# Optimization experiments

Measured on AMD Instinct MI355X. Metric: run time of the kernel, lower is better.

Reference implementation:

```python
import jax, jax.numpy as jnp
import numpy as np

N_NODES = 30000
N_EDGES = 480000
NODE_DIM = 16
NUM_RADIAL = 8
NUM_ELEMENTS = 120
R_MAX = 5.0
NUM_BLOCKS = 2
N_PATHS = 5  # h0*sh0->0e, h0*sh1->1o, h0*sh2->2e, h1.sh1->0e, h2.sh2->0e


def _sh_basis(u):
    # real spherical harmonics up to l=2, component normalization, on unit vectors u [E,3]
    x, y, z = u[:, 0], u[:, 1], u[:, 2]
    s15 = jnp.sqrt(jnp.asarray(15.0, u.dtype))
    s5 = jnp.sqrt(jnp.asarray(5.0, u.dtype))
    sh1 = jnp.sqrt(jnp.asarray(3.0, u.dtype)) * u                      # [E,3]
    sh2 = jnp.stack([s15 * x * y, s15 * y * z,
                     0.5 * s5 * (3.0 * z * z - 1.0),
                     s15 * x * z, 0.5 * s15 * (x * x - y * y)], -1)    # [E,5]
    return sh1, sh2


def _energy(pos, emb, W_init, Wr, br, W_out, W_read, W1, b1, W2, b2, z, edge_index):
    N = pos.shape[0]
    row, col = edge_index[0], edge_index[1]
    edge_vec = pos[row] - pos[col]                                     # [E,3] gather
    r = jnp.sqrt(jnp.sum(edge_vec * edge_vec, -1) + 1e-12)             # [E]
    n = jnp.arange(1, NUM_RADIAL + 1, dtype=pos.dtype)
    # Bessel radial basis: sqrt(2/rc) * sin(n*pi*r/rc)/r
    radial = jnp.sqrt(2.0 / R_MAX) * jnp.sin(n[None, :] * jnp.pi * r[:, None] / R_MAX) / r[:, None]  # [E,R]
    u = edge_vec / r[:, None]
    sh1, sh2 = _sh_basis(u)

    # initial projection: embedding scalars -> 0e channels; l=1,l=2 start at zero
    h0 = emb[z] @ W_init                                               # [N,C]
    h1 = jnp.zeros((N, NODE_DIM, 3), pos.dtype)
    h2 = jnp.zeros((N, NODE_DIM, 5), pos.dtype)

    for b in range(NUM_BLOCKS):
        w = (radial @ Wr[b] + br[b]).reshape(-1, N_PATHS, NODE_DIM)    # [E,P,C] radial path weights
        h0c, h1c, h2c = h0[col], h1[col], h2[col]
        # scalar messages: h0*sh0 + <h1,sh1> + <h2,sh2>
        m0 = (w[:, 0] * h0c
              + w[:, 3] * jnp.einsum('ecm,em->ec', h1c, sh1)
              + w[:, 4] * jnp.einsum('ecm,em->ec', h2c, sh2))          # [E,C]
        m1 = (w[:, 1] * h0c)[:, :, None] * sh1[:, None, :]             # [E,C,3]
        m2 = (w[:, 2] * h0c)[:, :, None] * sh2[:, None, :]             # [E,C,5]
        a0 = jax.ops.segment_sum(m0, row, num_segments=N)
        a1 = jax.ops.segment_sum(m1, row, num_segments=N)
        a2 = jax.ops.segment_sum(m2, row, num_segments=N)
        h0 = h0 + a0 @ W_out[b, 0]
        h1 = h1 + jnp.einsum('ncm,cd->ndm', a1, W_out[b, 1])
        h2 = h2 + jnp.einsum('ncm,cd->ndm', a2, W_out[b, 2])

    inv = h0 @ W_read                                                  # readout 0e part
    site = jax.nn.silu(inv @ W1 + b1) @ W2 + b2                        # [N,1]
    return jnp.sum(site)


def setup_inputs() -> dict:
    key = jax.random.key(0)
    ks = jax.random.split(key, 12)
    C, R = NODE_DIM, NUM_RADIAL
    s = 1.0 / np.sqrt(C)
    return {
        'pos': jax.random.normal(ks[0], (N_NODES, 3), jnp.float32) * 3.0,
        'z': jax.random.randint(ks[1], (N_NODES,), 0, NUM_ELEMENTS),
        'edge_index': jax.random.randint(ks[2], (2, N_EDGES), 0, N_NODES),
        'emb': jax.random.normal(ks[3], (NUM_ELEMENTS, C), jnp.float32),
        'W_init': jax.random.normal(ks[4], (C, C), jnp.float32) * s,
        'Wr': jax.random.normal(ks[5], (NUM_BLOCKS, R, N_PATHS * C), jnp.float32) / np.sqrt(R),
        'br': jnp.zeros((NUM_BLOCKS, N_PATHS * C), jnp.float32),
        'W_out': jax.random.normal(ks[6], (NUM_BLOCKS, 3, C, C), jnp.float32) * s,
        'W_read': jax.random.normal(ks[7], (C, C), jnp.float32) * s,
        'W1': jax.random.normal(ks[8], (C, C), jnp.float32) * s,
        'b1': jnp.zeros((C,), jnp.float32),
        'W2': jax.random.normal(ks[9], (C, 1), jnp.float32) * s,
        'b2': jnp.zeros((1,), jnp.float32),
    }


def reference(pos, z, edge_index, emb, W_init, Wr, br, W_out, W_read, W1, b1, W2, b2):
    e_fn = lambda p: _energy(p, emb, W_init, Wr, br, W_out, W_read, W1, b1, W2, b2, z, edge_index)
    total, dE_dpos = jax.value_and_grad(e_fn)(pos)
    energy = jnp.reshape(total, (1, 1))
    forces = -dE_dpos
    return energy, forces
```

## Files before the change

kernel.cpp:

```cpp
#include <hip/hip_runtime.h>
#include <math.h>

#ifndef M_PI
#define M_PI 3.14159265358979323846
#endif

static inline int cdiv(int a, int b){ return (a + b - 1) / b; }

#define SQRT3f  1.7320508075688772f
#define SQRT5f  2.23606797749979f
#define SQRT15f 3.872983346207417f
#define KRADf   0.6324555320336759f
#define PI5f    0.6283185307179586f
#define KPI5f   (KRADf * PI5f)
#define CSH2f   (0.5f*SQRT5f)
#define CSH4f   (0.5f*SQRT15f)


__device__ __forceinline__ float grp16_sum(float v){
  v += __shfl_xor(v, 1, 64);
  v += __shfl_xor(v, 2, 64);
  v += __shfl_xor(v, 4, 64);
  v += __shfl_xor(v, 8, 64);
  return v;
}
__device__ __forceinline__ float xgrp_sum(float v){
  v += __shfl_xor(v, 16, 64);
  v += __shfl_xor(v, 32, 64);
  return v;
}

__device__ __forceinline__ void base2_from_u(float ux, float uy, float uz, float* b2)
{
  float z2 = uz*uz, x2 = ux*ux, y2 = uy*uy;
  b2[0] = ux*uy;
  b2[1] = uy*uz;
  b2[2] = fmaf(z2, 3.f, -1.f);
  b2[3] = ux*uz;
  b2[4] = x2 - y2;
}


__global__ void k_hist(const int* __restrict__ ei, int E,
                       int* __restrict__ deg_row, int* __restrict__ deg_col)
{
  int e = blockIdx.x * blockDim.x + threadIdx.x;
  if (e >= E) return;
  atomicAdd(&deg_row[ei[e]], 1);
  atomicAdd(&deg_col[ei[E + e]], 1);
}

__global__ void k_alloc(const int* __restrict__ deg_row, const int* __restrict__ deg_col,
                        int* __restrict__ start_row, int* __restrict__ cur_row,
                        int* __restrict__ start_col, int* __restrict__ cur_col,
                        int* __restrict__ cursors, int N)
{
  int idx = blockIdx.x * blockDim.x + threadIdx.x;
  int lane = threadIdx.x & 63;
  #pragma unroll
  for (int which = 0; which < 2; which++) {
    const int* deg = which ? deg_col : deg_row;
    int* start = which ? start_col : start_row;
    int* cur   = which ? cur_col   : cur_row;
    int v = (idx < N) ? deg[idx] : 0;
    int incl = v;
    #pragma unroll
    for (int d = 1; d < 64; d <<= 1) {
      int y = __shfl_up(incl, d, 64);
      if (lane >= d) incl += y;
    }
    int wtot = __shfl(incl, 63, 64);
    int base = 0;
    if (lane == 63) base = atomicAdd(&cursors[which], wtot);
    base = __shfl(base, 63, 64);
    if (idx < N) { int st = base + incl - v; start[idx] = st; cur[idx] = st; }
  }
}

__global__ void k_scatter_geom(const float* __restrict__ pos, const int* __restrict__ ei, int E,
                               int* __restrict__ cur_row, int* __restrict__ cur_col,
                               float4* __restrict__ uR, float2* __restrict__ scR,
                               float4* __restrict__ uC, float2* __restrict__ scC,
                               int* __restrict__ colR, int* __restrict__ cposR,
                               int* __restrict__ rowC, int* __restrict__ rposC)
{
  int e = blockIdx.x * blockDim.x + threadIdx.x;
  if (e >= E) return;
  int row = ei[e], col = ei[E + e];
  int pr = atomicAdd(&cur_row[row], 1);
  int pc = atomicAdd(&cur_col[col], 1);
  colR[pr] = col; cposR[pr] = pc;
  rowC[pc] = row; rposC[pc] = pr;

  float px = pos[row*3+0] - pos[col*3+0];
  float py = pos[row*3+1] - pos[col*3+1];
  float pz = pos[row*3+2] - pos[col*3+2];
  float r2 = px*px + py*py + pz*pz + 1e-12f;
  float r = sqrtf(r2);
  float inv_r = 1.0f / r;
  float ux = px*inv_r, uy = py*inv_r, uz = pz*inv_r;
  float s1, c1;
  sincosf(r * PI5f, &s1, &c1);
  float4 u4 = make_float4(ux, uy, uz, inv_r);
  float2 sc = make_float2(s1, c1);
  uR[pr] = u4; scR[pr] = sc;
  uC[pc] = u4; scC[pc] = sc;
}

__global__ void k_node_init(const float* __restrict__ emb, const int* __restrict__ z,
                            const float* __restrict__ W_init, float* __restrict__ h0, int N)
{
  __shared__ float sW[256];
  if (threadIdx.x < 256) sW[threadIdx.x] = W_init[threadIdx.x];
  __syncthreads();
  int n = blockIdx.x * blockDim.x + threadIdx.x;
  if (n >= N) return;
  const float* e = emb + z[n]*16;
  float ev[16];
  #pragma unroll
  for (int k = 0; k < 16; k++) ev[k] = e[k];
  #pragma unroll
  for (int c = 0; c < 16; c++) {
    float s = 0.f;
    #pragma unroll
    for (int k = 0; k < 16; k++) s += ev[k] * sW[k*16+c];
    h0[n*16+c] = s;
  }
}

__global__ void k_fwd_b0(const float* __restrict__ Wr, const float* __restrict__ br,
                         const float* __restrict__ h0_in,
                         const float4* __restrict__ uR, const float2* __restrict__ scR,
                         const int* __restrict__ colR,
                         const int* __restrict__ start_row, const int* __restrict__ deg_row,
                         float* __restrict__ a0, float* __restrict__ a1, float* __restrict__ a2,
                         int N)
{
  int wid = (blockIdx.x * blockDim.x + threadIdx.x) >> 6;
  int nw  = (gridDim.x * blockDim.x) >> 6;
  int lane = threadIdx.x & 63;
  int g = lane >> 4, c = lane & 15;
  float wr0[8], wr1[8], wr2[8];
  #pragma unroll
  for (int k = 0; k < 8; k++) {
    wr0[k] = Wr[k*80 + c];
    wr1[k] = Wr[k*80 + 16 + c];
    wr2[k] = Wr[k*80 + 32 + c];
  }
  float b0v = br[c], b1v = br[16 + c], b2v = br[32 + c];

  for (int n = wid; n < N; n += nw) {
    float acc0 = 0.f, acc1[3] = {0.f,0.f,0.f}, acc2[5] = {0.f,0.f,0.f,0.f,0.f};

    int i0 = start_row[n] + g, i1 = start_row[n] + deg_row[n];
    float4 Un = {0,0,0,0}; float2 SCn = {0,0};
    float h0n = 0.f;
    if (i0 < i1) {
      Un = uR[i0]; SCn = scR[i0];
      h0n = h0_in[colR[i0]*16 + c];
    }
    for (int i = i0; i < i1; i += 4) {
      float4 U = Un; float2 SC = SCn;
      float h0c = h0n;
      if (i+4 < i1) {
        Un = uR[i+4]; SCn = scR[i+4];
        h0n = h0_in[colR[i+4]*16 + c];
      }
      float Ki = KRADf * U.w;
      float tc = 2.f * SC.y;
      float sprev = 0.f, s = SC.x;
      float w0 = b0v, w1 = b1v, w2 = b2v;
      #pragma unroll
      for (int k = 0; k < 8; k++) {
        float rad = Ki * s;
        w0 += rad*wr0[k]; w1 += rad*wr1[k]; w2 += rad*wr2[k];
        float sn = tc*s - sprev; sprev = s; s = sn;
      }
      float b2[5];
      base2_from_u(U.x, U.y, U.z, b2);
      acc0 += w0*h0c;
      float wh1 = w1*h0c, wh2 = w2*h0c;
      acc1[0] += wh1*U.x; acc1[1] += wh1*U.y; acc1[2] += wh1*U.z;
      #pragma unroll
      for (int m = 0; m < 5; m++) acc2[m] += wh2*b2[m];
    }
    acc0 = xgrp_sum(acc0);
    #pragma unroll
    for (int m = 0; m < 3; m++) acc1[m] = xgrp_sum(acc1[m]);
    #pragma unroll
    for (int m = 0; m < 5; m++) acc2[m] = xgrp_sum(acc2[m]);
    if (g == 0) {
      a0[n*16 + c] = acc0;
      a1[n*48 + c*3 + 0] = SQRT3f*acc1[0];
      a1[n*48 + c*3 + 1] = SQRT3f*acc1[1];
      a1[n*48 + c*3 + 2] = SQRT3f*acc1[2];
      a2[n*80 + c*5 + 0] = SQRT15f*acc2[0];
      a2[n*80 + c*5 + 1] = SQRT15f*acc2[1];
      a2[n*80 + c*5 + 2] = CSH2f  *acc2[2];
      a2[n*80 + c*5 + 3] = SQRT15f*acc2[3];
      a2[n*80 + c*5 + 4] = CSH4f  *acc2[4];
    }
  }
}

__global__ void k_fwd_b1(const float* __restrict__ Wr, const float* __restrict__ br,
                         const float* __restrict__ h0_in, const float* __restrict__ h1_in,
                         const float* __restrict__ h2_in,
                         const float4* __restrict__ uR, const float2* __restrict__ scR,
                         const int* __restrict__ colR,
                         const int* __restrict__ start_row, const int* __restrict__ deg_row,
                         float* __restrict__ a0, int N)
{
  int wid = (blockIdx.x * blockDim.x + threadIdx.x) >> 6;
  int nw  = (gridDim.x * blockDim.x) >> 6;
  int lane = threadIdx.x & 63;
  int g = lane >> 4, c = lane & 15;
  float wr0[8], wr3[8], wr4[8];
  #pragma unroll
  for (int k = 0; k < 8; k++) {
    wr0[k] = Wr[k*80 + c];
    wr3[k] = SQRT3f*Wr[k*80 + 48 + c];
    wr4[k] = Wr[k*80 + 64 + c];
  }
  float b0v = br[c], b3v = SQRT3f*br[48 + c], b4v = br[64 + c];

  for (int n = wid; n < N; n += nw) {
    float acc0 = 0.f;
    int i0 = start_row[n] + g, i1 = start_row[n] + deg_row[n];
    float4 Un = {0,0,0,0}; float2 SCn = {0,0};
    float h0n = 0.f, h1n[3] = {0,0,0}, h2n[5] = {0,0,0,0,0};
    if (i0 < i1) {
      int col = colR[i0];
      Un = uR[i0]; SCn = scR[i0];
      h0n = h0_in[col*16 + c];
      #pragma unroll
      for (int m = 0; m < 3; m++) h1n[m] = h1_in[col*48 + c*3 + m];
      #pragma unroll
      for (int m = 0; m < 5; m++) h2n[m] = h2_in[col*80 + c*5 + m];
    }
    for (int i = i0; i < i1; i += 4) {
      float4 U = Un; float2 SC = SCn;
      float h0c = h0n;
      float h1c[3], h2c[5];
      #pragma unroll
      for (int m = 0; m < 3; m++) h1c[m] = h1n[m];
      #pragma unroll
      for (int m = 0; m < 5; m++) h2c[m] = h2n[m];
      if (i+4 < i1) {
        int col = colR[i+4];
        Un = uR[i+4]; SCn = scR[i+4];
        h0n = h0_in[col*16 + c];
        #pragma unroll
        for (int m = 0; m < 3; m++) h1n[m] = h1_in[col*48 + c*3 + m];
        #pragma unroll
        for (int m = 0; m < 5; m++) h2n[m] = h2_in[col*80 + c*5 + m];
      }
      float Ki = KRADf * U.w;
      float tc = 2.f * SC.y;
      float sprev = 0.f, s = SC.x;
      float w0 = b0v, w3 = b3v, w4 = b4v;
      #pragma unroll
      for (int k = 0; k < 8; k++) {
        float rad = Ki * s;
        w0 += rad*wr0[k]; w3 += rad*wr3[k]; w4 += rad*wr4[k];
        float sn = tc*s - sprev; sprev = s; s = sn;
      }
      float b2[5];
      base2_from_u(U.x, U.y, U.z, b2);
      float S1 = h1c[0]*U.x + h1c[1]*U.y + h1c[2]*U.z;
      float A  = h2c[0]*b2[0] + h2c[1]*b2[1] + h2c[3]*b2[3];
      float B  = CSH2f*(h2c[2]*b2[2]) + CSH4f*(h2c[4]*b2[4]);
      float S2 = fmaf(SQRT15f, A, B);
      acc0 += w0*h0c + w3*S1 + w4*S2;
    }
    acc0 = xgrp_sum(acc0);
    if (g == 0) a0[n*16 + c] = acc0;
  }
}

__global__ void k_node_update(const float* __restrict__ h0_in,
                              const float* __restrict__ a0, const float* __restrict__ a1,
                              const float* __restrict__ a2,
                              const float* __restrict__ U,
                              float* __restrict__ h0_out, float* __restrict__ h1_out,
                              float* __restrict__ h2_out, int N)
{
  int idx = blockIdx.x * blockDim.x + threadIdx.x;
  int n = idx >> 4, d = idx & 15;
  if (n >= N) return;
  const float* U0 = U;
  const float* U1 = U + 256;
  const float* U2 = U + 512;
  float s = h0_in[n*16 + d];
  #pragma unroll
  for (int c = 0; c < 16; c++) s += a0[n*16 + c] * U0[c*16 + d];
  h0_out[n*16 + d] = s;
  float v1[3] = {0.f, 0.f, 0.f};
  #pragma unroll
  for (int c = 0; c < 16; c++) {
    float u = U1[c*16 + d];
    #pragma unroll
    for (int m = 0; m < 3; m++) v1[m] += a1[n*48 + c*3 + m] * u;
  }
  #pragma unroll
  for (int m = 0; m < 3; m++) h1_out[n*48 + d*3 + m] = v1[m];
  float v2[5] = {0.f, 0.f, 0.f, 0.f, 0.f};
  #pragma unroll
  for (int c = 0; c < 16; c++) {
    float u = U2[c*16 + d];
    #pragma unroll
    for (int m = 0; m < 5; m++) v2[m] += a2[n*80 + c*5 + m] * u;
  }
  #pragma unroll
  for (int m = 0; m < 5; m++) h2_out[n*80 + d*5 + m] = v2[m];
}

__global__ void __launch_bounds__(256, 1)
k_readout_bwd(const float* __restrict__ h0s1, const float* __restrict__ a0in,
              const float* __restrict__ W_read,
              const float* __restrict__ W1, const float* __restrict__ b1,
              const float* __restrict__ W2, const float* __restrict__ b2,
              const float* __restrict__ U0b1,
              float* __restrict__ g0, float* __restrict__ ga0,
              float* __restrict__ partials, int N)
{
  __shared__ float sWr[256], sW1[256], sU[256], sb1[16], sW2[16], sb2;
  __shared__ float swave[4];
  {
    int t = threadIdx.x;
    if (t < 256) { sWr[t] = W_read[t]; sW1[t] = W1[t]; sU[t] = U0b1[t]; }
    if (t < 16)  { sb1[t] = b1[t]; sW2[t] = W2[t]; }
    if (t == 0)  sb2 = b2[0];
  }
  __syncthreads();
  int n = blockIdx.x * blockDim.x + threadIdx.x;
  float site = 0.f;
  if (n < N) {
    float h[16], av[16], inv[16], dt[16], g0v[16];
    #pragma unroll
    for (int d = 0; d < 16; d++) av[d] = a0in[n*16 + d];
    #pragma unroll
    for (int d = 0; d < 16; d++) {
      float s = h0s1[n*16 + d];
      #pragma unroll
      for (int cc = 0; cc < 16; cc++) s += av[cc] * sU[cc*16 + d];
      h[d] = s;
    }
    #pragma unroll
    for (int j = 0; j < 16; j++) {
      float s = 0.f;
      #pragma unroll
      for (int d = 0; d < 16; d++) s += h[d] * sWr[d*16 + j];
      inv[j] = s;
    }
    site = sb2;
    #pragma unroll
    for (int c = 0; c < 16; c++) {
      float t = sb1[c];
      #pragma unroll
      for (int j = 0; j < 16; j++) t += inv[j] * sW1[j*16 + c];
      float sg = 1.f / (1.f + expf(-t));
      float w2v = sW2[c];
      site += t * sg * w2v;
      dt[c] = w2v * sg * (1.f + t * (1.f - sg));
    }
    float dinv[16];
    #pragma unroll
    for (int j = 0; j < 16; j++) {
      float s = 0.f;
      #pragma unroll
      for (int c = 0; c < 16; c++) s += dt[c] * sW1[j*16 + c];
      dinv[j] = s;
    }
    #pragma unroll
    for (int d = 0; d < 16; d++) {
      float s = 0.f;
      #pragma unroll
      for (int j = 0; j < 16; j++) s += dinv[j] * sWr[d*16 + j];
      g0v[d] = s;
      g0[n*16 + d] = s;
    }
    #pragma unroll
    for (int c = 0; c < 16; c++) {
      float s = 0.f;
      #pragma unroll
      for (int d = 0; d < 16; d++) s += g0v[d] * sU[c*16 + d];
      ga0[n*16 + c] = s;
    }
  }
  #pragma unroll
  for (int off = 32; off; off >>= 1) site += __shfl_down(site, off, 64);
  int wave = threadIdx.x >> 6;
  if ((threadIdx.x & 63) == 0) swave[wave] = site;
  __syncthreads();
  if (threadIdx.x == 0)
    partials[blockIdx.x] = swave[0] + swave[1] + swave[2] + swave[3];
}

__global__ void k_energy(const float* __restrict__ partials, int nb,
                         float* __restrict__ energy)
{
  int t = threadIdx.x;
  float s = 0.f;
  for (int i = t; i < nb; i += 128) s += partials[i];
  #pragma unroll
  for (int off = 32; off; off >>= 1) s += __shfl_down(s, off, 64);
  __shared__ float sw[2];
  if ((t & 63) == 0) sw[t >> 6] = s;
  __syncthreads();
  if (t == 0) energy[0] = sw[0] + sw[1];
}

__global__ void k_ga(const float* __restrict__ g0, const float* __restrict__ g1,
                     const float* __restrict__ g2, const float* __restrict__ U,
                     float* __restrict__ ga0, float* __restrict__ ga1, float* __restrict__ ga2,
                     int N)
{
  int idx = blockIdx.x * blockDim.x + threadIdx.x;
  int n = idx >> 4, c = idx & 15;
  if (n >= N) return;
  const float* U0 = U;
  const float* U1 = U + 256;
  const float* U2 = U + 512;
  float s = 0.f;
  #pragma unroll
  for (int d = 0; d < 16; d++) s += g0[n*16 + d] * U0[c*16 + d];
  ga0[n*16 + c] = s;
  float v1[3] = {0.f, 0.f, 0.f};
  #pragma unroll
  for (int d = 0; d < 16; d++) {
    float u = U1[c*16 + d];
    #pragma unroll
    for (int m = 0; m < 3; m++) v1[m] += g1[n*48 + d*3 + m] * u;
  }
  #pragma unroll
  for (int m = 0; m < 3; m++) ga1[n*48 + c*3 + m] = v1[m];
  float v2[5] = {0.f, 0.f, 0.f, 0.f, 0.f};
  #pragma unroll
  for (int d = 0; d < 16; d++) {
    float u = U2[c*16 + d];
    #pragma unroll
    for (int m = 0; m < 5; m++) v2[m] += g2[n*80 + d*5 + m] * u;
  }
  #pragma unroll
  for (int m = 0; m < 5; m++) ga2[n*80 + c*5 + m] = v2[m];
}

__global__ void k_bwd_b1_col(const float* __restrict__ Wr, const float* __restrict__ br,
                             const float* __restrict__ h0_in, const float* __restrict__ h1_in,
                             const float* __restrict__ h2_in,
                             const float* __restrict__ ga0,
                             const float4* __restrict__ uC, const float2* __restrict__ scC,
                             const int* __restrict__ rowC,
                             const int* __restrict__ start_col, const int* __restrict__ deg_col,
                             float* __restrict__ g0, float* __restrict__ g1, float* __restrict__ g2,
                             float* __restrict__ dv_col, int N)
{
  int wid = (blockIdx.x * blockDim.x + threadIdx.x) >> 6;
  int nw  = (gridDim.x * blockDim.x) >> 6;
  int lane = threadIdx.x & 63;
  int g = lane >> 4, c = lane & 15;
  float wr0[8], wr3[8], wr4[8];
  #pragma unroll
  for (int k = 0; k < 8; k++) {
    wr0[k] = Wr[k*80 + c];
    wr3[k] = Wr[k*80 + 48 + c];
    wr4[k] = Wr[k*80 + 64 + c];
  }
  float b0v = br[c], b3v = br[48 + c], b4v = br[64 + c];

  for (int n = wid; n < N; n += nw) {
    float h0c = h0_in[n*16 + c];
    float h1s[3], h2s[5];
    #pragma unroll
    for (int m = 0; m < 3; m++) h1s[m] = SQRT3f * h1_in[n*48 + c*3 + m];
    h2s[0] = SQRT15f * h2_in[n*80 + c*5 + 0];
    h2s[1] = SQRT15f * h2_in[n*80 + c*5 + 1];
    h2s[2] = CSH2f   * h2_in[n*80 + c*5 + 2];
    h2s[3] = SQRT15f * h2_in[n*80 + c*5 + 3];
    h2s[4] = CSH4f   * h2_in[n*80 + c*5 + 4];

    float accg0 = 0.f, accg1[3] = {0.f,0.f,0.f}, accg2[5] = {0.f,0.f,0.f,0.f,0.f};

    int i0 = start_col[n] + g, i1 = start_col[n] + deg_col[n];
    float4 Un = {0,0,0,0}; float2 SCn = {0,0};
    float dm0n = 0.f;
    if (i0 < i1) {
      Un = uC[i0]; SCn = scC[i0];
      dm0n = ga0[rowC[i0]*16 + c];
    }
    for (int i = i0; i < i1; i += 4) {
      float4 U = Un; float2 SC = SCn;
      float dm0 = dm0n;
      if (i+4 < i1) {
        Un = uC[i+4]; SCn = scC[i+4];
        dm0n = ga0[rowC[i+4]*16 + c];
      }
      float ux = U.x, uy = U.y, uz = U.z, inv_r = U.w;
      float b2[5];
      base2_from_u(ux, uy, uz, b2);

      float S1 = h1s[0]*ux + h1s[1]*uy + h1s[2]*uz;
      float S2 = h2s[0]*b2[0] + h2s[1]*b2[1] + h2s[2]*b2[2]
               + h2s[3]*b2[3] + h2s[4]*b2[4];

      float dw0 = dm0 * h0c;
      float dw3 = dm0 * S1;
      float dw4 = dm0 * S2;

      float Ki = KRADf * inv_r;
      float tcv = 2.f * SC.y;
      float sprev = 0.f, s = SC.x, cprev = 1.f, cc = SC.y;
      float w0 = b0v, w3 = b3v, w4 = b4v;
      float P = 0.f, Q = 0.f;
      #pragma unroll
      for (int k = 0; k < 8; k++) {
        float rad = Ki * s;
        w0 += rad*wr0[k]; w3 += rad*wr3[k]; w4 += rad*wr4[k];
        float t = dw0*wr0[k] + dw3*wr3[k] + dw4*wr4[k];
        P = fmaf(t*cc, (float)(k+1), P);
        Q = fmaf(t, rad, Q);
        float sn = tcv*s - sprev; sprev = s; s = sn;
        float cn = tcv*cc - cprev; cprev = cc; cc = cn;
      }

      float t3 = dm0 * w3, t4 = dm0 * w4;
      accg0 += dm0 * w0;
      accg1[0] += t3*ux; accg1[1] += t3*uy; accg1[2] += t3*uz;
      #pragma unroll
      for (int m = 0; m < 5; m++) accg2[m] += t4*b2[m];

      float q1x = t3*h1s[0], q1y = t3*h1s[1], q1z = t3*h1s[2];
      float q0 = t4*h2s[0], q1 = t4*h2s[1], q2 = t4*h2s[2], q3 = t4*h2s[3], q4 = t4*h2s[4];
      float q4d = q4 + q4;
      float q2h = 6.f*q2;
      float gr = (KPI5f*P - Q) * inv_r;
      float gux = q1x + uy*q0 + uz*q3 + ux*q4d;
      float guy = q1y + ux*q0 + uz*q1 - uy*q4d;
      float guz = q1z + uy*q1 + uz*q2h + ux*q3;

      gr  = grp16_sum(gr);
      gux = grp16_sum(gux);
      guy = grp16_sum(guy);
      guz = grp16_sum(guz);

      if (c == 0) {
        float gdotu = gux*ux + guy*uy + guz*uz;
        dv_col[i*3+0] = gr*ux + (gux - gdotu*ux)*inv_r;
        dv_col[i*3+1] = gr*uy + (guy - gdotu*uy)*inv_r;
        dv_col[i*3+2] = gr*uz + (guz - gdotu*uz)*inv_r;
      }
    }
    accg0 = xgrp_sum(accg0);
    #pragma unroll
    for (int m = 0; m < 3; m++) accg1[m] = xgrp_sum(accg1[m]);
    #pragma unroll
    for (int m = 0; m < 5; m++) accg2[m] = xgrp_sum(accg2[m]);
    if (g == 0) {
      g0[n*16 + c] += accg0;
      g1[n*48 + c*3 + 0] = SQRT3f*accg1[0];
      g1[n*48 + c*3 + 1] = SQRT3f*accg1[1];
      g1[n*48 + c*3 + 2] = SQRT3f*accg1[2];
      g2[n*80 + c*5 + 0] = SQRT15f*accg2[0];
      g2[n*80 + c*5 + 1] = SQRT15f*accg2[1];
      g2[n*80 + c*5 + 2] = CSH2f  *accg2[2];
      g2[n*80 + c*5 + 3] = SQRT15f*accg2[3];
      g2[n*80 + c*5 + 4] = CSH4f  *accg2[4];
    }
  }
}

__global__ void k_bwd_b0_row(const float* __restrict__ Wr, const float* __restrict__ br,
                             const float* __restrict__ h0_in,
                             const float* __restrict__ ga0, const float* __restrict__ ga1,
                             const float* __restrict__ ga2,
                             const float4* __restrict__ uR, const float2* __restrict__ scR,
                             const int* __restrict__ colR,
                             const int* __restrict__ start_row, const int* __restrict__ deg_row,
                             float* __restrict__ dv_row, int N)
{
  int wid = (blockIdx.x * blockDim.x + threadIdx.x) >> 6;
  int nw  = (gridDim.x * blockDim.x) >> 6;
  int lane = threadIdx.x & 63;
  int g = lane >> 4, c = lane & 15;
  float wr0[8], wr1[8], wr2[8];
  #pragma unroll
  for (int k = 0; k < 8; k++) {
    wr0[k] = Wr[k*80 + c];
    wr1[k] = Wr[k*80 + 16 + c];
    wr2[k] = Wr[k*80 + 32 + c];
  }
  float b1v = br[16 + c], b2v = br[32 + c];

  for (int n = wid; n < N; n += nw) {
    float dm0 = ga0[n*16 + c];
    float dm1s[3], dm2s[5];
    #pragma unroll
    for (int m = 0; m < 3; m++) dm1s[m] = SQRT3f * ga1[n*48 + c*3 + m];
    dm2s[0] = SQRT15f * ga2[n*80 + c*5 + 0];
    dm2s[1] = SQRT15f * ga2[n*80 + c*5 + 1];
    dm2s[2] = CSH2f   * ga2[n*80 + c*5 + 2];
    dm2s[3] = SQRT15f * ga2[n*80 + c*5 + 3];
    dm2s[4] = CSH4f   * ga2[n*80 + c*5 + 4];

    int i0 = start_row[n] + g, i1 = start_row[n] + deg_row[n];
    float4 Un = {0,0,0,0}; float2 SCn = {0,0};
    float h0n = 0.f;
    if (i0 < i1) {
      Un = uR[i0]; SCn = scR[i0];
      h0n = h0_in[colR[i0]*16 + c];
    }
    for (int i = i0; i < i1; i += 4) {
      float4 U = Un; float2 SC = SCn;
      float h0c = h0n;
      if (i+4 < i1) {
        Un = uR[i+4]; SCn = scR[i+4];
        h0n = h0_in[colR[i+4]*16 + c];
      }
      float ux = U.x, uy = U.y, uz = U.z, inv_r = U.w;
      float b2[5];
      base2_from_u(ux, uy, uz, b2);

      float T1 = dm1s[0]*ux + dm1s[1]*uy + dm1s[2]*uz;
      float T2 = dm2s[0]*b2[0] + dm2s[1]*b2[1] + dm2s[2]*b2[2]
               + dm2s[3]*b2[3] + dm2s[4]*b2[4];

      float dw0 = dm0 * h0c;
      float dw1 = h0c * T1;
      float dw2 = h0c * T2;

      float Ki = KRADf * inv_r;
      float tcv = 2.f * SC.y;
      float sprev = 0.f, s = SC.x, cprev = 1.f, cc = SC.y;
      float w1 = b1v, w2v = b2v;
      float P = 0.f, Q = 0.f;
      #pragma unroll
      for (int k = 0; k < 8; k++) {
        float rad = Ki * s;
        w1 += rad*wr1[k]; w2v += rad*wr2[k];
        float t = dw0*wr0[k] + dw1*wr1[k] + dw2*wr2[k];
        P = fmaf(t*cc, (float)(k+1), P);
        Q = fmaf(t, rad, Q);
        float sn = tcv*s - sprev; sprev = s; s = sn;
        float cn2 = tcv*cc - cprev; cprev = cc; cc = cn2;
      }

      float w1h = w1*h0c, w2h = w2v*h0c;
      float q1x = dm1s[0]*w1h, q1y = dm1s[1]*w1h, q1z = dm1s[2]*w1h;
      float q0 = dm2s[0]*w2h, q1 = dm2s[1]*w2h, q2 = dm2s[2]*w2h, q3 = dm2s[3]*w2h, q4 = dm2s[4]*w2h;
      float q4d = q4 + q4;
      float q2h = 6.f*q2;
      float gr = (KPI5f*P - Q) * inv_r;
      float gux = q1x + uy*q0 + uz*q3 + ux*q4d;
      float guy = q1y + ux*q0 + uz*q1 - uy*q4d;
      float guz = q1z + uy*q1 + uz*q2h + ux*q3;

      gr  = grp16_sum(gr);
      gux = grp16_sum(gux);
      guy = grp16_sum(guy);
      guz = grp16_sum(guz);

      if (c == 0) {
        float gdotu = gux*ux + guy*uy + guz*uz;
        dv_row[i*3+0] = gr*ux + (gux - gdotu*ux)*inv_r;
        dv_row[i*3+1] = gr*uy + (guy - gdotu*uy)*inv_r;
        dv_row[i*3+2] = gr*uz + (guz - gdotu*uz)*inv_r;
      }
    }
  }
}

__global__ void k_force(const int* __restrict__ start_row, const int* __restrict__ deg_row,
                        const int* __restrict__ cposR,
                        const int* __restrict__ start_col, const int* __restrict__ deg_col,
                        const int* __restrict__ rposC,
                        const float* __restrict__ dv_col, const float* __restrict__ dv_row,
                        float* __restrict__ force, int N)
{
  int idx = blockIdx.x * blockDim.x + threadIdx.x;
  int n = idx >> 4, l = idx & 15;
  if (n >= N) return;
  float fx = 0.f, fy = 0.f, fz = 0.f;
  int c0 = start_col[n], c1 = c0 + deg_col[n];
  for (int i = c0 + l; i < c1; i += 16) {
    int rp = rposC[i];
    fx += dv_col[i*3+0] + dv_row[rp*3+0];
    fy += dv_col[i*3+1] + dv_row[rp*3+1];
    fz += dv_col[i*3+2] + dv_row[rp*3+2];
  }
  int r0 = start_row[n], r1 = r0 + deg_row[n];
  for (int i = r0 + l; i < r1; i += 16) {
    int cp = cposR[i];
    fx -= dv_row[i*3+0] + dv_col[cp*3+0];
    fy -= dv_row[i*3+1] + dv_col[cp*3+1];
    fz -= dv_row[i*3+2] + dv_col[cp*3+2];
  }
  fx = grp16_sum(fx); fy = grp16_sum(fy); fz = grp16_sum(fz);
  if (l == 0) {
    force[n*3+0] = fx; force[n*3+1] = fy; force[n*3+2] = fz;
  }
}

extern "C" void kernel_launch(void* const* d_in, const int* in_sizes, int n_in,
                              void* d_out, int out_size, void* d_ws, size_t ws_size,
                              hipStream_t stream)
{
  const float* pos    = (const float*)d_in[0];
  const int*   z      = (const int*)  d_in[1];
  const int*   ei     = (const int*)  d_in[2];
  const float* emb    = (const float*)d_in[3];
  const float* W_init = (const float*)d_in[4];
  const float* Wr     = (const float*)d_in[5];
  const float* br     = (const float*)d_in[6];
  const float* W_out  = (const float*)d_in[7];
  const float* W_read = (const float*)d_in[8];
  const float* W1     = (const float*)d_in[9];
  const float* b1     = (const float*)d_in[10];
  const float* W2     = (const float*)d_in[11];
  const float* b2     = (const float*)d_in[12];

  const int N = in_sizes[0] / 3;
  const int E = in_sizes[2] / 2;

  const int BLK = 256;
  const int NB_READOUT = cdiv(N, BLK);
  const int PBLK = (N < 8192) ? cdiv(N, 4) : 2048;

  float* f = (float*)d_ws;
  float4* uR  = (float4*)f; f += (size_t)E*4;
  float4* uC  = (float4*)f; f += (size_t)E*4;
  float2* scR = (float2*)f; f += (size_t)E*2;
  float2* scC = (float2*)f; f += (size_t)E*2;
  float* h0_s0 = f; f += (size_t)N*16;
  float* h0_s1 = f; f += (size_t)N*16;
  float* h1_s1 = f; f += (size_t)N*48;
  float* h2_s1 = f; f += (size_t)N*80;
  float* a0    = f; f += (size_t)N*16;
  float* a1    = f; f += (size_t)N*48;
  float* a2    = f; f += (size_t)N*80;
  float* ga0b1 = f; f += (size_t)N*16;
  float* g0    = f; f += (size_t)N*16;
  float* g1    = f; f += (size_t)N*48;
  float* g2    = f; f += (size_t)N*80;
  float* dv_c  = f; f += (size_t)E*3;
  float* dv_r  = f; f += (size_t)E*3;
  float* partials = f; f += (size_t)NB_READOUT;
  int* ip = (int*)f;
  int* cursors   = ip; ip += 2;
  int* deg_row   = ip; ip += N;
  int* deg_col   = ip; ip += N;
  int* start_row = ip; ip += N;
  int* start_col = ip; ip += N;
  int* cur_row   = ip; ip += N;
  int* cur_col   = ip; ip += N;
  int* colR      = ip; ip += E;
  int* cposR     = ip; ip += E;
  int* rowC      = ip; ip += E;
  int* rposC     = ip; ip += E;

  float* out    = (float*)d_out;
  float* energy = out;
  float* force  = out + 1;

  (void)hipMemsetAsync(cursors, 0, (size_t)(2 + 2*N) * sizeof(int), stream);

  k_hist<<<cdiv(E, BLK), BLK, 0, stream>>>(ei, E, deg_row, deg_col);
  k_alloc<<<cdiv(N, BLK), BLK, 0, stream>>>(deg_row, deg_col, start_row, cur_row,
                                            start_col, cur_col, cursors, N);
  k_scatter_geom<<<cdiv(E, BLK), BLK, 0, stream>>>(pos, ei, E, cur_row, cur_col,
                                                   uR, scR, uC, scC,
                                                   colR, cposR, rowC, rposC);

  k_node_init<<<cdiv(N, BLK), BLK, 0, stream>>>(emb, z, W_init, h0_s0, N);

  k_fwd_b0<<<PBLK, BLK, 0, stream>>>(Wr, br, h0_s0, uR, scR, colR,
                                     start_row, deg_row, a0, a1, a2, N);
  k_node_update<<<cdiv(N*16, BLK), BLK, 0, stream>>>(h0_s0, a0, a1, a2,
                                                     W_out, h0_s1, h1_s1, h2_s1, N);

  k_fwd_b1<<<PBLK, BLK, 0, stream>>>(Wr + 640, br + 80,
                                     h0_s1, h1_s1, h2_s1, uR, scR, colR,
                                     start_row, deg_row, a0, N);

  k_readout_bwd<<<NB_READOUT, BLK, 0, stream>>>(h0_s1, a0, W_read, W1, b1, W2, b2,
                                                W_out + 768, g0, ga0b1, partials, N);
  k_energy<<<1, 128, 0, stream>>>(partials, NB_READOUT, energy);

  k_bwd_b1_col<<<PBLK, BLK, 0, stream>>>(Wr + 640, br + 80,
                                         h0_s1, h1_s1, h2_s1, ga0b1,
                                         uC, scC, rowC, start_col, deg_col,
                                         g0, g1, g2, dv_c, N);

  k_ga<<<cdiv(N*16, BLK), BLK, 0, stream>>>(g0, g1, g2, W_out, a0, a1, a2, N);
  k_bwd_b0_row<<<PBLK, BLK, 0, stream>>>(Wr, br, h0_s0,
                                         a0, a1, a2, uR, scR, colR,
                                         start_row, deg_row, dv_r, N);

  k_force<<<cdiv(N*16, BLK), BLK, 0, stream>>>(start_row, deg_row, cposR,
                                               start_col, deg_col, rposC,
                                               dv_c, dv_r, force, N);
}
```

Baseline: 469.6 us.

## Fuse node-update and gradient-transform matmuls into edge aggregation kernels

The per-node W_out channel mixing is folded into the tail of the forward block-0 aggregation kernel, and the backward W_out^T mixing into the tail of the block-1 column kernel. Both use wave shuffles plus a shared-memory copy of W_out, so the separate k_node_update and k_ga launches and the a/g intermediate round trips through global memory disappear. The neighbour index is also loaded one iteration further ahead to deepen the gather prefetch. The cost is extra shuffle and reduction work at the end of each node, plus higher register pressure in the fused kernels.

Measured after the change: 455.7 us. 1.03x faster.

```diff
diff --git a/kernel.cpp b/kernel.cpp
--- a/kernel.cpp
+++ b/kernel.cpp
@@ -39,7 +39,6 @@
   b2[3] = ux*uz;
   b2[4] = x2 - y2;
 }
-
 
 __global__ void k_hist(const int* __restrict__ ei, int E,
                        int* __restrict__ deg_row, int* __restrict__ deg_col)
@@ -133,8 +132,472 @@
                          const float4* __restrict__ uR, const float2* __restrict__ scR,
                          const int* __restrict__ colR,
                          const int* __restrict__ start_row, const int* __restrict__ deg_row,
-                         float* __restrict__ a0, float* __restrict__ a1, float* __restrict__ a2,
-                         int N)
+                         const float* __restrict__ U,
+                         float* __restrict__ h0_out, float* __restrict__ h1_out,
+                         float* __restrict__ h2_out, int N)
+{
+  __shared__ float sU[768];
+  for (int t = threadIdx.x; t < 768; t += blockDim.x) sU[t] = U[t];
+  __syncthreads();
+
+  int wid = (blockIdx.x * blockDim.x + threadIdx.x) >> 6;
+  int nw  = (gridDim.x * blockDim.x) >> 6;
+  int lane = threadIdx.x & 63;
+  int g = lane >> 4, c = lane & 15;
+  int gbase = lane & 48;
+  float wr0[8], wr1[8], wr2[8];
+  #pragma unroll
+  for (int k = 0; k < 8; k++) {
+    wr0[k] = Wr[k*80 + c];
+    wr1[k] = Wr[k*80 + 16 + c];
+    wr2[k] = Wr[k*80 + 32 + c];
+  }
+  float b0v = br[c], b1v = br[16 + c], b2v = br[32 + c];
+
+  for (int n = wid; n < N; n += nw) {
+    float acc0 = 0.f, acc1[3] = {0.f,0.f,0.f}, acc2[5] = {0.f,0.f,0.f,0.f,0.f};
+
+    int i0 = start_row[n] + g, i1 = start_row[n] + deg_row[n];
+    float4 Un = {0,0,0,0}; float2 SCn = {0,0};
+    float h0n = 0.f; int cB = 0;
+    if (i0 < i1) {
+      int cA = colR[i0];
+      cB = (i0+4 < i1) ? colR[i0+4] : 0;
+      Un = uR[i0]; SCn = scR[i0];
+      h0n = h0_in[cA*16 + c];
+    }
+    for (int i = i0; i < i1; i += 4) {
+      float4 U4 = Un; float2 SC = SCn;
+      float h0c = h0n;
+      if (i+4 < i1) {
+        Un = uR[i+4]; SCn = scR[i+4];
+        h0n = h0_in[cB*16 + c];
+        cB = (i+8 < i1) ? colR[i+8] : 0;
+      }
+      float Ki = KRADf * U4.w;
+      float tc = 2.f * SC.y;
+      float sprev = 0.f, s = SC.x;
+      float w0 = b0v, w1 = b1v, w2 = b2v;
+      #pragma unroll
+      for (int k = 0; k < 8; k++) {
+        float rad = Ki * s;
+        w0 += rad*wr0[k]; w1 += rad*wr1[k]; w2 += rad*wr2[k];
+        float sn = tc*s - sprev; sprev = s; s = sn;
+      }
+      float b2m[5];
+      base2_from_u(U4.x, U4.y, U4.z, b2m);
+      acc0 += w0*h0c;
+      float wh1 = w1*h0c, wh2 = w2*h0c;
+      acc1[0] += wh1*U4.x; acc1[1] += wh1*U4.y; acc1[2] += wh1*U4.z;
+      #pragma unroll
+      for (int m = 0; m < 5; m++) acc2[m] += wh2*b2m[m];
+    }
+    acc0 = xgrp_sum(acc0);
+    #pragma unroll
+    for (int m = 0; m < 3; m++) acc1[m] = xgrp_sum(acc1[m]);
+    #pragma unroll
+    for (int m = 0; m < 5; m++) acc2[m] = xgrp_sum(acc2[m]);
+
+    float o0 = 0.f, o1[3] = {0.f,0.f,0.f}, o2[5] = {0.f,0.f,0.f,0.f,0.f};
+    #pragma unroll
+    for (int j = 0; j < 4; j++) {
+      int cs = (g << 2) + j;
+      int sl = gbase + cs;
+      float a0b  = __shfl(acc0, sl, 64);
+      float a1b0 = __shfl(acc1[0], sl, 64);
+      float a1b1 = __shfl(acc1[1], sl, 64);
+      float a1b2 = __shfl(acc1[2], sl, 64);
+      float a2b0 = __shfl(acc2[0], sl, 64);
+      float a2b1 = __shfl(acc2[1], sl, 64);
+      float a2b2 = __shfl(acc2[2], sl, 64);
+      float a2b3 = __shfl(acc2[3], sl, 64);
+      float a2b4 = __shfl(acc2[4], sl, 64);
+      float u0v = sU[cs*16 + c];
+      float u1v = sU[256 + cs*16 + c];
+      float u2v = sU[512 + cs*16 + c];
+      o0 += a0b*u0v;
+      o1[0] += a1b0*u1v; o1[1] += a1b1*u1v; o1[2] += a1b2*u1v;
+      o2[0] += a2b0*u2v; o2[1] += a2b1*u2v; o2[2] += a2b2*u2v;
+      o2[3] += a2b3*u2v; o2[4] += a2b4*u2v;
+    }
+    o0 = xgrp_sum(o0);
+    #pragma unroll
+    for (int m = 0; m < 3; m++) o1[m] = xgrp_sum(o1[m]);
+    #pragma unroll
+    for (int m = 0; m < 5; m++) o2[m] = xgrp_sum(o2[m]);
+    if (g == 0) {
+      h0_out[n*16 + c] = h0_in[n*16 + c] + o0;
+    } else if (g == 1) {
+      h1_out[n*48 + c*3 + 0] = SQRT3f*o1[0];
+      h1_out[n*48 + c*3 + 1] = SQRT3f*o1[1];
+      h1_out[n*48 + c*3 + 2] = SQRT3f*o1[2];
+    } else if (g == 2) {
+      h2_out[n*80 + c*5 + 0] = SQRT15f*o2[0];
+      h2_out[n*80 + c*5 + 1] = SQRT15f*o2[1];
+      h2_out[n*80 + c*5 + 2] = CSH2f  *o2[2];
+    } else {
+      h2_out[n*80 + c*5 + 3] = SQRT15f*o2[3];
+      h2_out[n*80 + c*5 + 4] = CSH4f  *o2[4];
+    }
+  }
+}
+
+__global__ void k_fwd_b1(const float* __restrict__ Wr, const float* __restrict__ br,
+                         const float* __restrict__ h0_in, const float* __restrict__ h1_in,
+                         const float* __restrict__ h2_in,
+                         const float4* __restrict__ uR, const float2* __restrict__ scR,
+                         const int* __restrict__ colR,
+                         const int* __restrict__ start_row, const int* __restrict__ deg_row,
+                         float* __restrict__ a0, int N)
+{
+  int wid = (blockIdx.x * blockDim.x + threadIdx.x) >> 6;
+  int nw  = (gridDim.x * blockDim.x) >> 6;
+  int lane = threadIdx.x & 63;
+  int g = lane >> 4, c = lane & 15;
+  float wr0[8], wr3[8], wr4[8];
+  #pragma unroll
+  for (int k = 0; k < 8; k++) {
+    wr0[k] = Wr[k*80 + c];
+    wr3[k] = SQRT3f*Wr[k*80 + 48 + c];
+    wr4[k] = Wr[k*80 + 64 + c];
+  }
+  float b0v = br[c], b3v = SQRT3f*br[48 + c], b4v = br[64 + c];
+
+  for (int n = wid; n < N; n += nw) {
+    float acc0 = 0.f;
+    int i0 = start_row[n] + g, i1 = start_row[n] + deg_row[n];
+    float4 Un = {0,0,0,0}; float2 SCn = {0,0};
+    float h0n = 0.f, h1n[3] = {0,0,0}, h2n[5] = {0,0,0,0,0};
+    int cB = 0;
+    if (i0 < i1) {
+      int cA = colR[i0];
+      cB = (i0+4 < i1) ? colR[i0+4] : 0;
+      Un = uR[i0]; SCn = scR[i0];
+      h0n = h0_in[cA*16 + c];
+      #pragma unroll
+      for (int m = 0; m < 3; m++) h1n[m] = h1_in[cA*48 + c*3 + m];
+      #pragma unroll
+      for (int m = 0; m < 5; m++) h2n[m] = h2_in[cA*80 + c*5 + m];
+    }
+    for (int i = i0; i < i1; i += 4) {
+      float4 U = Un; float2 SC = SCn;
+      float h0c = h0n;
+      float h1c[3], h2c[5];
+      #pragma unroll
+      for (int m = 0; m < 3; m++) h1c[m] = h1n[m];
+      #pragma unroll
+      for (int m = 0; m < 5; m++) h2c[m] = h2n[m];
+      if (i+4 < i1) {
+        Un = uR[i+4]; SCn = scR[i+4];
+        h0n = h0_in[cB*16 + c];
+        #pragma unroll
+        for (int m = 0; m < 3; m++) h1n[m] = h1_in[cB*48 + c*3 + m];
+        #pragma unroll
+        for (int m = 0; m < 5; m++) h2n[m] = h2_in[cB*80 + c*5 + m];
+        cB = (i+8 < i1) ? colR[i+8] : 0;
+      }
+      float Ki = KRADf * U.w;
+      float tc = 2.f * SC.y;
+      float sprev = 0.f, s = SC.x;
+      float w0 = b0v, w3 = b3v, w4 = b4v;
+      #pragma unroll
+      for (int k = 0; k < 8; k++) {
+        float rad = Ki * s;
+        w0 += rad*wr0[k]; w3 += rad*wr3[k]; w4 += rad*wr4[k];
+        float sn = tc*s - sprev; sprev = s; s = sn;
+      }
+      float b2[5];
+      base2_from_u(U.x, U.y, U.z, b2);
+      float S1 = h1c[0]*U.x + h1c[1]*U.y + h1c[2]*U.z;
+      float A  = h2c[0]*b2[0] + h2c[1]*b2[1] + h2c[3]*b2[3];
+      float B  = CSH2f*(h2c[2]*b2[2]) + CSH4f*(h2c[4]*b2[4]);
+      float S2 = fmaf(SQRT15f, A, B);
+      acc0 += w0*h0c + w3*S1 + w4*S2;
+    }
+    acc0 = xgrp_sum(acc0);
+    if (g == 0) a0[n*16 + c] = acc0;
+  }
+}
+
+__global__ void __launch_bounds__(256, 1)
+k_readout_bwd(const float* __restrict__ h0s1, const float* __restrict__ a0in,
+              const float* __restrict__ W_read,
+              const float* __restrict__ W1, const float* __restrict__ b1,
+              const float* __restrict__ W2, const float* __restrict__ b2,
+              const float* __restrict__ U0b1,
+              float* __restrict__ g0, float* __restrict__ ga0,
+              float* __restrict__ partials, int N)
+{
+  __shared__ float sWr[256], sW1[256], sU[256], sb1[16], sW2[16], sb2;
+  __shared__ float swave[4];
+  {
+    int t = threadIdx.x;
+    if (t < 256) { sWr[t] = W_read[t]; sW1[t] = W1[t]; sU[t] = U0b1[t]; }
+    if (t < 16)  { sb1[t] = b1[t]; sW2[t] = W2[t]; }
+    if (t == 0)  sb2 = b2[0];
+  }
+  __syncthreads();
+  int n = blockIdx.x * blockDim.x + threadIdx.x;
+  float site = 0.f;
+  if (n < N) {
+    float h[16], av[16], inv[16], dt[16], g0v[16];
+    #pragma unroll
+    for (int d = 0; d < 16; d++) av[d] = a0in[n*16 + d];
+    #pragma unroll
+    for (int d = 0; d < 16; d++) {
+      float s = h0s1[n*16 + d];
+      #pragma unroll
+      for (int cc = 0; cc < 16; cc++) s += av[cc] * sU[cc*16 + d];
+      h[d] = s;
+    }
+    #pragma unroll
+    for (int j = 0; j < 16; j++) {
+      float s = 0.f;
+      #pragma unroll
+      for (int d = 0; d < 16; d++) s += h[d] * sWr[d*16 + j];
+      inv[j] = s;
+    }
+    site = sb2;
+    #pragma unroll
+    for (int c = 0; c < 16; c++) {
+      float t = sb1[c];
+      #pragma unroll
+      for (int j = 0; j < 16; j++) t += inv[j] * sW1[j*16 + c];
+      float sg = 1.f / (1.f + expf(-t));
+      float w2v = sW2[c];
+      site += t * sg * w2v;
+      dt[c] = w2v * sg * (1.f + t * (1.f - sg));
+    }
+    float dinv[16];
+    #pragma unroll
+    for (int j = 0; j < 16; j++) {
+      float s = 0.f;
+      #pragma unroll
+      for (int c = 0; c < 16; c++) s += dt[c] * sW1[j*16 + c];
+      dinv[j] = s;
+    }
+    #pragma unroll
+    for (int d = 0; d < 16; d++) {
+      float s = 0.f;
+      #pragma unroll
+      for (int j = 0; j < 16; j++) s += dinv[j] * sWr[d*16 + j];
+      g0v[d] = s;
+      g0[n*16 + d] = s;
+    }
+    #pragma unroll
+    for (int c = 0; c < 16; c++) {
+      float s = 0.f;
+      #pragma unroll
+      for (int d = 0; d < 16; d++) s += g0v[d] * sU[c*16 + d];
+      ga0[n*16 + c] = s;
+    }
+  }
+  #pragma unroll
+  for (int off = 32; off; off >>= 1) site += __shfl_down(site, off, 64);
+  int wave = threadIdx.x >> 6;
+  if ((threadIdx.x & 63) == 0) swave[wave] = site;
+  __syncthreads();
+  if (threadIdx.x == 0)
+    partials[blockIdx.x] = swave[0] + swave[1] + swave[2] + swave[3];
+}
+
+__global__ void k_energy(const float* __restrict__ partials, int nb,
+                         float* __restrict__ energy)
+{
+  int t = threadIdx.x;
+  float s = 0.f;
+  for (int i = t; i < nb; i += 128) s += partials[i];
+  #pragma unroll
+  for (int off = 32; off; off >>= 1) s += __shfl_down(s, off, 64);
+  __shared__ float sw[2];
+  if ((t & 63) == 0) sw[t >> 6] = s;
+  __syncthreads();
+  if (t == 0) energy[0] = sw[0] + sw[1];
+}
+
+__global__ void k_bwd_b1_col(const float* __restrict__ Wr, const float* __restrict__ br,
+                             const float* __restrict__ h0_in, const float* __restrict__ h1_in,
+                             const float* __restrict__ h2_in,
+                             const float* __restrict__ ga0,
+                             const float4* __restrict__ uC, const float2* __restrict__ scC,
+                             const int* __restrict__ rowC,
+                             const int* __restrict__ start_col, const int* __restrict__ deg_col,
+                             const float* __restrict__ g0_in,
+                             const float* __restrict__ U,
+                             float* __restrict__ gaout0, float* __restrict__ gaout1,
+                             float* __restrict__ gaout2,
+                             float* __restrict__ dv_col, int N)
+{
+  __shared__ float sUT[768];
+  {
+    int t = threadIdx.x;
+    if (t < 256) {
+      int cc = t & 15, dd = t >> 4;
+      sUT[dd*16 + cc]       = U[cc*16 + dd];
+      sUT[256 + dd*16 + cc] = U[256 + cc*16 + dd];
+      sUT[512 + dd*16 + cc] = U[512 + cc*16 + dd];
+    }
+  }
+  __syncthreads();
+
+  int wid = (blockIdx.x * blockDim.x + threadIdx.x) >> 6;
+  int nw  = (gridDim.x * blockDim.x) >> 6;
+  int lane = threadIdx.x & 63;
+  int g = lane >> 4, c = lane & 15;
+  int gbase = lane & 48;
+  float wr0[8], wr3[8], wr4[8];
+  #pragma unroll
+  for (int k = 0; k < 8; k++) {
+    wr0[k] = Wr[k*80 + c];
+    wr3[k] = Wr[k*80 + 48 + c];
+    wr4[k] = Wr[k*80 + 64 + c];
+  }
+  float b0v = br[c], b3v = br[48 + c], b4v = br[64 + c];
+
+  for (int n = wid; n < N; n += nw) {
+    float h0c = h0_in[n*16 + c];
+    float h1s[3], h2s[5];
+    #pragma unroll
+    for (int m = 0; m < 3; m++) h1s[m] = SQRT3f * h1_in[n*48 + c*3 + m];
+    h2s[0] = SQRT15f * h2_in[n*80 + c*5 + 0];
+    h2s[1] = SQRT15f * h2_in[n*80 + c*5 + 1];
+    h2s[2] = CSH2f   * h2_in[n*80 + c*5 + 2];
+    h2s[3] = SQRT15f * h2_in[n*80 + c*5 + 3];
+    h2s[4] = CSH4f   * h2_in[n*80 + c*5 + 4];
+
+    float accg0 = 0.f, accg1[3] = {0.f,0.f,0.f}, accg2[5] = {0.f,0.f,0.f,0.f,0.f};
+
+    int i0 = start_col[n] + g, i1 = start_col[n] + deg_col[n];
+    float4 Un = {0,0,0,0}; float2 SCn = {0,0};
+    float dm0n = 0.f; int rB = 0;
+    if (i0 < i1) {
+      int rA = rowC[i0];
+      rB = (i0+4 < i1) ? rowC[i0+4] : 0;
+      Un = uC[i0]; SCn = scC[i0];
+      dm0n = ga0[rA*16 + c];
+    }
+    for (int i = i0; i < i1; i += 4) {
+      float4 U4 = Un; float2 SC = SCn;
+      float dm0 = dm0n;
+      if (i+4 < i1) {
+        Un = uC[i+4]; SCn = scC[i+4];
+        dm0n = ga0[rB*16 + c];
+        rB = (i+8 < i1) ? rowC[i+8] : 0;
+      }
+      float ux = U4.x, uy = U4.y, uz = U4.z, inv_r = U4.w;
+      float b2[5];
+      base2_from_u(ux, uy, uz, b2);
+
+      float S1 = h1s[0]*ux + h1s[1]*uy + h1s[2]*uz;
+      float S2 = h2s[0]*b2[0] + h2s[1]*b2[1] + h2s[2]*b2[2]
+               + h2s[3]*b2[3] + h2s[4]*b2[4];
+
+      float dw0 = dm0 * h0c;
+      float dw3 = dm0 * S1;
+      float dw4 = dm0 * S2;
+
+      float Ki = KRADf * inv_r;
+      float tcv = 2.f * SC.y;
+      float sprev = 0.f, s = SC.x, cprev = 1.f, cc = SC.y;
+      float w0 = b0v, w3 = b3v, w4 = b4v;
+      float P = 0.f, Q = 0.f;
+      #pragma unroll
+      for (int k = 0; k < 8; k++) {
+        float rad = Ki * s;
+        w0 += rad*wr0[k]; w3 += rad*wr3[k]; w4 += rad*wr4[k];
+        float t = dw0*wr0[k] + dw3*wr3[k] + dw4*wr4[k];
+        P = fmaf(t*cc, (float)(k+1), P);
+        Q = fmaf(t, rad, Q);
+        float sn = tcv*s - sprev; sprev = s; s = sn;
+        float cn = tcv*cc - cprev; cprev = cc; cc = cn;
+      }
+
+      float t3 = dm0 * w3, t4 = dm0 * w4;
+      accg0 += dm0 * w0;
+      accg1[0] += t3*ux; accg1[1] += t3*uy; accg1[2] += t3*uz;
+      #pragma unroll
+      for (int m = 0; m < 5; m++) accg2[m] += t4*b2[m];
+
+      float q1x = t3*h1s[0], q1y = t3*h1s[1], q1z = t3*h1s[2];
+      float q0 = t4*h2s[0], q1 = t4*h2s[1], q2 = t4*h2s[2], q3 = t4*h2s[3], q4 = t4*h2s[4];
+      float q4d = q4 + q4;
+      float q2h = 6.f*q2;
+      float gr = (KPI5f*P - Q) * inv_r;
+      float gux = q1x + uy*q0 + uz*q3 + ux*q4d;
+      float guy = q1y + ux*q0 + uz*q1 - uy*q4d;
+      float guz = q1z + uy*q1 + uz*q2h + ux*q3;
+
+      gr  = grp16_sum(gr);
+      gux = grp16_sum(gux);
+      guy = grp16_sum(guy);
+      guz = grp16_sum(guz);
+
+      if (c == 0) {
+        float gdotu = gux*ux + guy*uy + guz*uz;
+        dv_col[i*3+0] = gr*ux + (gux - gdotu*ux)*inv_r;
+        dv_col[i*3+1] = gr*uy + (guy - gdotu*uy)*inv_r;
+        dv_col[i*3+2] = gr*uz + (guz - gdotu*uz)*inv_r;
+      }
+    }
+    accg0 = xgrp_sum(accg0);
+    #pragma unroll
+    for (int m = 0; m < 3; m++) accg1[m] = xgrp_sum(accg1[m]);
+    #pragma unroll
+    for (int m = 0; m < 5; m++) accg2[m] = xgrp_sum(accg2[m]);
+
+    float t0 = g0_in[n*16 + c] + accg0;
+    float o0 = 0.f, o1[3] = {0.f,0.f,0.f}, o2[5] = {0.f,0.f,0.f,0.f,0.f};
+    #pragma unroll
+    for (int j = 0; j < 4; j++) {
+      int ds = (g << 2) + j;
+      int sl = gbase + ds;
+      float b0  = __shfl(t0, sl, 64);
+      float b10 = __shfl(accg1[0], sl, 64);
+      float b11 = __shfl(accg1[1], sl, 64);
+      float b12 = __shfl(accg1[2], sl, 64);
+      float b20 = __shfl(accg2[0], sl, 64);
+      float b21 = __shfl(accg2[1], sl, 64);
+      float b22 = __shfl(accg2[2], sl, 64);
+      float b23 = __shfl(accg2[3], sl, 64);
+      float b24 = __shfl(accg2[4], sl, 64);
+      float ut0 = sUT[ds*16 + c];
+      float ut1 = sUT[256 + ds*16 + c];
+      float ut2 = sUT[512 + ds*16 + c];
+      o0 += b0*ut0;
+      o1[0] += b10*ut1; o1[1] += b11*ut1; o1[2] += b12*ut1;
+      o2[0] += b20*ut2; o2[1] += b21*ut2; o2[2] += b22*ut2;
+      o2[3] += b23*ut2; o2[4] += b24*ut2;
+    }
+    o0 = xgrp_sum(o0);
+    #pragma unroll
+    for (int m = 0; m < 3; m++) o1[m] = xgrp_sum(o1[m]);
+    #pragma unroll
+    for (int m = 0; m < 5; m++) o2[m] = xgrp_sum(o2[m]);
+    if (g == 0) {
+      gaout0[n*16 + c] = o0;
+    } else if (g == 1) {
+      gaout1[n*48 + c*3 + 0] = SQRT3f*o1[0];
+      gaout1[n*48 + c*3 + 1] = SQRT3f*o1[1];
+      gaout1[n*48 + c*3 + 2] = SQRT3f*o1[2];
+    } else if (g == 2) {
+      gaout2[n*80 + c*5 + 0] = SQRT15f*o2[0];
+      gaout2[n*80 + c*5 + 1] = SQRT15f*o2[1];
+      gaout2[n*80 + c*5 + 2] = CSH2f  *o2[2];
+    } else {
+      gaout2[n*80 + c*5 + 3] = SQRT15f*o2[3];
+      gaout2[n*80 + c*5 + 4] = CSH4f  *o2[4];
+    }
+  }
+}
+
+__global__ void k_bwd_b0_row(const float* __restrict__ Wr, const float* __restrict__ br,
+                             const float* __restrict__ h0_in,
+                             const float* __restrict__ ga0, const float* __restrict__ ga1,
+                             const float* __restrict__ ga2,
+                             const float4* __restrict__ uR, const float2* __restrict__ scR,
+                             const int* __restrict__ colR,
+                             const int* __restrict__ start_row, const int* __restrict__ deg_row,
+                             float* __restrict__ dv_row, int N)
 {
   int wid = (blockIdx.x * blockDim.x + threadIdx.x) >> 6;
   int nw  = (gridDim.x * blockDim.x) >> 6;
@@ -147,449 +610,6 @@
     wr1[k] = Wr[k*80 + 16 + c];
     wr2[k] = Wr[k*80 + 32 + c];
   }
-  float b0v = br[c], b1v = br[16 + c], b2v = br[32 + c];
-
-  for (int n = wid; n < N; n += nw) {
-    float acc0 = 0.f, acc1[3] = {0.f,0.f,0.f}, acc2[5] = {0.f,0.f,0.f,0.f,0.f};
-
-    int i0 = start_row[n] + g, i1 = start_row[n] + deg_row[n];
-    float4 Un = {0,0,0,0}; float2 SCn = {0,0};
-    float h0n = 0.f;
-    if (i0 < i1) {
-      Un = uR[i0]; SCn = scR[i0];
-      h0n = h0_in[colR[i0]*16 + c];
-    }
-    for (int i = i0; i < i1; i += 4) {
-      float4 U = Un; float2 SC = SCn;
-      float h0c = h0n;
-      if (i+4 < i1) {
-        Un = uR[i+4]; SCn = scR[i+4];
-        h0n = h0_in[colR[i+4]*16 + c];
-      }
-      float Ki = KRADf * U.w;
-      float tc = 2.f * SC.y;
-      float sprev = 0.f, s = SC.x;
-      float w0 = b0v, w1 = b1v, w2 = b2v;
-      #pragma unroll
-      for (int k = 0; k < 8; k++) {
-        float rad = Ki * s;
-        w0 += rad*wr0[k]; w1 += rad*wr1[k]; w2 += rad*wr2[k];
-        float sn = tc*s - sprev; sprev = s; s = sn;
-      }
-      float b2[5];
-      base2_from_u(U.x, U.y, U.z, b2);
-      acc0 += w0*h0c;
-      float wh1 = w1*h0c, wh2 = w2*h0c;
-      acc1[0] += wh1*U.x; acc1[1] += wh1*U.y; acc1[2] += wh1*U.z;
-      #pragma unroll
-      for (int m = 0; m < 5; m++) acc2[m] += wh2*b2[m];
-    }
-    acc0 = xgrp_sum(acc0);
-    #pragma unroll
-    for (int m = 0; m < 3; m++) acc1[m] = xgrp_sum(acc1[m]);
-    #pragma unroll
-    for (int m = 0; m < 5; m++) acc2[m] = xgrp_sum(acc2[m]);
-    if (g == 0) {
-      a0[n*16 + c] = acc0;
-      a1[n*48 + c*3 + 0] = SQRT3f*acc1[0];
-      a1[n*48 + c*3 + 1] = SQRT3f*acc1[1];
-      a1[n*48 + c*3 + 2] = SQRT3f*acc1[2];
-      a2[n*80 + c*5 + 0] = SQRT15f*acc2[0];
-      a2[n*80 + c*5 + 1] = SQRT15f*acc2[1];
-      a2[n*80 + c*5 + 2] = CSH2f  *acc2[2];
-      a2[n*80 + c*5 + 3] = SQRT15f*acc2[3];
-      a2[n*80 + c*5 + 4] = CSH4f  *acc2[4];
-    }
-  }
-}
-
-__global__ void k_fwd_b1(const float* __restrict__ Wr, const float* __restrict__ br,
-                         const float* __restrict__ h0_in, const float* __restrict__ h1_in,
-                         const float* __restrict__ h2_in,
-                         const float4* __restrict__ uR, const float2* __restrict__ scR,
-                         const int* __restrict__ colR,
-                         const int* __restrict__ start_row, const int* __restrict__ deg_row,
-                         float* __restrict__ a0, int N)
-{
-  int wid = (blockIdx.x * blockDim.x + threadIdx.x) >> 6;
-  int nw  = (gridDim.x * blockDim.x) >> 6;
-  int lane = threadIdx.x & 63;
-  int g = lane >> 4, c = lane & 15;
-  float wr0[8], wr3[8], wr4[8];
-  #pragma unroll
-  for (int k = 0; k < 8; k++) {
-    wr0[k] = Wr[k*80 + c];
-    wr3[k] = SQRT3f*Wr[k*80 + 48 + c];
-    wr4[k] = Wr[k*80 + 64 + c];
-  }
-  float b0v = br[c], b3v = SQRT3f*br[48 + c], b4v = br[64 + c];
-
-  for (int n = wid; n < N; n += nw) {
-    float acc0 = 0.f;
-    int i0 = start_row[n] + g, i1 = start_row[n] + deg_row[n];
-    float4 Un = {0,0,0,0}; float2 SCn = {0,0};
-    float h0n = 0.f, h1n[3] = {0,0,0}, h2n[5] = {0,0,0,0,0};
-    if (i0 < i1) {
-      int col = colR[i0];
-      Un = uR[i0]; SCn = scR[i0];
-      h0n = h0_in[col*16 + c];
-      #pragma unroll
-      for (int m = 0; m < 3; m++) h1n[m] = h1_in[col*48 + c*3 + m];
-      #pragma unroll
-      for (int m = 0; m < 5; m++) h2n[m] = h2_in[col*80 + c*5 + m];
-    }
-    for (int i = i0; i < i1; i += 4) {
-      float4 U = Un; float2 SC = SCn;
-      float h0c = h0n;
-      float h1c[3], h2c[5];
-      #pragma unroll
-      for (int m = 0; m < 3; m++) h1c[m] = h1n[m];
-      #pragma unroll
-      for (int m = 0; m < 5; m++) h2c[m] = h2n[m];
-      if (i+4 < i1) {
-        int col = colR[i+4];
-        Un = uR[i+4]; SCn = scR[i+4];
-        h0n = h0_in[col*16 + c];
-        #pragma unroll
-        for (int m = 0; m < 3; m++) h1n[m] = h1_in[col*48 + c*3 + m];
-        #pragma unroll
-        for (int m = 0; m < 5; m++) h2n[m] = h2_in[col*80 + c*5 + m];
-      }
-      float Ki = KRADf * U.w;
-      float tc = 2.f * SC.y;
-      float sprev = 0.f, s = SC.x;
-      float w0 = b0v, w3 = b3v, w4 = b4v;
-      #pragma unroll
-      for (int k = 0; k < 8; k++) {
-        float rad = Ki * s;
-        w0 += rad*wr0[k]; w3 += rad*wr3[k]; w4 += rad*wr4[k];
-        float sn = tc*s - sprev; sprev = s; s = sn;
-      }
-      float b2[5];
-      base2_from_u(U.x, U.y, U.z, b2);
-      float S1 = h1c[0]*U.x + h1c[1]*U.y + h1c[2]*U.z;
-      float A  = h2c[0]*b2[0] + h2c[1]*b2[1] + h2c[3]*b2[3];
-      float B  = CSH2f*(h2c[2]*b2[2]) + CSH4f*(h2c[4]*b2[4]);
-      float S2 = fmaf(SQRT15f, A, B);
-      acc0 += w0*h0c + w3*S1 + w4*S2;
-    }
-    acc0 = xgrp_sum(acc0);
-    if (g == 0) a0[n*16 + c] = acc0;
-  }
-}
-
-__global__ void k_node_update(const float* __restrict__ h0_in,
-                              const float* __restrict__ a0, const float* __restrict__ a1,
-                              const float* __restrict__ a2,
-                              const float* __restrict__ U,
-                              float* __restrict__ h0_out, float* __restrict__ h1_out,
-                              float* __restrict__ h2_out, int N)
-{
-  int idx = blockIdx.x * blockDim.x + threadIdx.x;
-  int n = idx >> 4, d = idx & 15;
-  if (n >= N) return;
-  const float* U0 = U;
-  const float* U1 = U + 256;
-  const float* U2 = U + 512;
-  float s = h0_in[n*16 + d];
-  #pragma unroll
-  for (int c = 0; c < 16; c++) s += a0[n*16 + c] * U0[c*16 + d];
-  h0_out[n*16 + d] = s;
-  float v1[3] = {0.f, 0.f, 0.f};
-  #pragma unroll
-  for (int c = 0; c < 16; c++) {
-    float u = U1[c*16 + d];
-    #pragma unroll
-    for (int m = 0; m < 3; m++) v1[m] += a1[n*48 + c*3 + m] * u;
-  }
-  #pragma unroll
-  for (int m = 0; m < 3; m++) h1_out[n*48 + d*3 + m] = v1[m];
-  float v2[5] = {0.f, 0.f, 0.f, 0.f, 0.f};
-  #pragma unroll
-  for (int c = 0; c < 16; c++) {
-    float u = U2[c*16 + d];
-    #pragma unroll
-    for (int m = 0; m < 5; m++) v2[m] += a2[n*80 + c*5 + m] * u;
-  }
-  #pragma unroll
-  for (int m = 0; m < 5; m++) h2_out[n*80 + d*5 + m] = v2[m];
-}
-
-__global__ void __launch_bounds__(256, 1)
-k_readout_bwd(const float* __restrict__ h0s1, const float* __restrict__ a0in,
-              const float* __restrict__ W_read,
-              const float* __restrict__ W1, const float* __restrict__ b1,
-              const float* __restrict__ W2, const float* __restrict__ b2,
-              const float* __restrict__ U0b1,
-              float* __restrict__ g0, float* __restrict__ ga0,
-              float* __restrict__ partials, int N)
-{
-  __shared__ float sWr[256], sW1[256], sU[256], sb1[16], sW2[16], sb2;
-  __shared__ float swave[4];
-  {
-    int t = threadIdx.x;
-    if (t < 256) { sWr[t] = W_read[t]; sW1[t] = W1[t]; sU[t] = U0b1[t]; }
-    if (t < 16)  { sb1[t] = b1[t]; sW2[t] = W2[t]; }
-    if (t == 0)  sb2 = b2[0];
-  }
-  __syncthreads();
-  int n = blockIdx.x * blockDim.x + threadIdx.x;
-  float site = 0.f;
-  if (n < N) {
-    float h[16], av[16], inv[16], dt[16], g0v[16];
-    #pragma unroll
-    for (int d = 0; d < 16; d++) av[d] = a0in[n*16 + d];
-    #pragma unroll
-    for (int d = 0; d < 16; d++) {
-      float s = h0s1[n*16 + d];
-      #pragma unroll
-      for (int cc = 0; cc < 16; cc++) s += av[cc] * sU[cc*16 + d];
-      h[d] = s;
-    }
-    #pragma unroll
-    for (int j = 0; j < 16; j++) {
-      float s = 0.f;
-      #pragma unroll
-      for (int d = 0; d < 16; d++) s += h[d] * sWr[d*16 + j];
-      inv[j] = s;
-    }
-    site = sb2;
-    #pragma unroll
-    for (int c = 0; c < 16; c++) {
-      float t = sb1[c];
-      #pragma unroll
-      for (int j = 0; j < 16; j++) t += inv[j] * sW1[j*16 + c];
-      float sg = 1.f / (1.f + expf(-t));
-      float w2v = sW2[c];
-      site += t * sg * w2v;
-      dt[c] = w2v * sg * (1.f + t * (1.f - sg));
-    }
-    float dinv[16];
-    #pragma unroll
-    for (int j = 0; j < 16; j++) {
-      float s = 0.f;
-      #pragma unroll
-      for (int c = 0; c < 16; c++) s += dt[c] * sW1[j*16 + c];
-      dinv[j] = s;
-    }
-    #pragma unroll
-    for (int d = 0; d < 16; d++) {
-      float s = 0.f;
-      #pragma unroll
-      for (int j = 0; j < 16; j++) s += dinv[j] * sWr[d*16 + j];
-      g0v[d] = s;
-      g0[n*16 + d] = s;
-    }
-    #pragma unroll
-    for (int c = 0; c < 16; c++) {
-      float s = 0.f;
-      #pragma unroll
-      for (int d = 0; d < 16; d++) s += g0v[d] * sU[c*16 + d];
-      ga0[n*16 + c] = s;
-    }
-  }
-  #pragma unroll
-  for (int off = 32; off; off >>= 1) site += __shfl_down(site, off, 64);
-  int wave = threadIdx.x >> 6;
-  if ((threadIdx.x & 63) == 0) swave[wave] = site;
-  __syncthreads();
-  if (threadIdx.x == 0)
-    partials[blockIdx.x] = swave[0] + swave[1] + swave[2] + swave[3];
-}
-
-__global__ void k_energy(const float* __restrict__ partials, int nb,
-                         float* __restrict__ energy)
-{
-  int t = threadIdx.x;
-  float s = 0.f;
-  for (int i = t; i < nb; i += 128) s += partials[i];
-  #pragma unroll
-  for (int off = 32; off; off >>= 1) s += __shfl_down(s, off, 64);
-  __shared__ float sw[2];
-  if ((t & 63) == 0) sw[t >> 6] = s;
-  __syncthreads();
-  if (t == 0) energy[0] = sw[0] + sw[1];
-}
-
-__global__ void k_ga(const float* __restrict__ g0, const float* __restrict__ g1,
-                     const float* __restrict__ g2, const float* __restrict__ U,
-                     float* __restrict__ ga0, float* __restrict__ ga1, float* __restrict__ ga2,
-                     int N)
-{
-  int idx = blockIdx.x * blockDim.x + threadIdx.x;
-  int n = idx >> 4, c = idx & 15;
-  if (n >= N) return;
-  const float* U0 = U;
-  const float* U1 = U + 256;
-  const float* U2 = U + 512;
-  float s = 0.f;
-  #pragma unroll
-  for (int d = 0; d < 16; d++) s += g0[n*16 + d] * U0[c*16 + d];
-  ga0[n*16 + c] = s;
-  float v1[3] = {0.f, 0.f, 0.f};
-  #pragma unroll
-  for (int d = 0; d < 16; d++) {
-    float u = U1[c*16 + d];
-    #pragma unroll
-    for (int m = 0; m < 3; m++) v1[m] += g1[n*48 + d*3 + m] * u;
-  }
-  #pragma unroll
-  for (int m = 0; m < 3; m++) ga1[n*48 + c*3 + m] = v1[m];
-  float v2[5] = {0.f, 0.f, 0.f, 0.f, 0.f};
-  #pragma unroll
-  for (int d = 0; d < 16; d++) {
-    float u = U2[c*16 + d];
-    #pragma unroll
-    for (int m = 0; m < 5; m++) v2[m] += g2[n*80 + d*5 + m] * u;
-  }
-  #pragma unroll
-  for (int m = 0; m < 5; m++) ga2[n*80 + c*5 + m] = v2[m];
-}
-
-__global__ void k_bwd_b1_col(const float* __restrict__ Wr, const float* __restrict__ br,
-                             const float* __restrict__ h0_in, const float* __restrict__ h1_in,
-                             const float* __restrict__ h2_in,
-                             const float* __restrict__ ga0,
-                             const float4* __restrict__ uC, const float2* __restrict__ scC,
-                             const int* __restrict__ rowC,
-                             const int* __restrict__ start_col, const int* __restrict__ deg_col,
-                             float* __restrict__ g0, float* __restrict__ g1, float* __restrict__ g2,
-                             float* __restrict__ dv_col, int N)
-{
-  int wid = (blockIdx.x * blockDim.x + threadIdx.x) >> 6;
-  int nw  = (gridDim.x * blockDim.x) >> 6;
-  int lane = threadIdx.x & 63;
-  int g = lane >> 4, c = lane & 15;
-  float wr0[8], wr3[8], wr4[8];
-  #pragma unroll
-  for (int k = 0; k < 8; k++) {
-    wr0[k] = Wr[k*80 + c];
-    wr3[k] = Wr[k*80 + 48 + c];
-    wr4[k] = Wr[k*80 + 64 + c];
-  }
-  float b0v = br[c], b3v = br[48 + c], b4v = br[64 + c];
-
-  for (int n = wid; n < N; n += nw) {
-    float h0c = h0_in[n*16 + c];
-    float h1s[3], h2s[5];
-    #pragma unroll
-    for (int m = 0; m < 3; m++) h1s[m] = SQRT3f * h1_in[n*48 + c*3 + m];
-    h2s[0] = SQRT15f * h2_in[n*80 + c*5 + 0];
-    h2s[1] = SQRT15f * h2_in[n*80 + c*5 + 1];
-    h2s[2] = CSH2f   * h2_in[n*80 + c*5 + 2];
-    h2s[3] = SQRT15f * h2_in[n*80 + c*5 + 3];
-    h2s[4] = CSH4f   * h2_in[n*80 + c*5 + 4];
-
-    float accg0 = 0.f, accg1[3] = {0.f,0.f,0.f}, accg2[5] = {0.f,0.f,0.f,0.f,0.f};
-
-    int i0 = start_col[n] + g, i1 = start_col[n] + deg_col[n];
-    float4 Un = {0,0,0,0}; float2 SCn = {0,0};
-    float dm0n = 0.f;
-    if (i0 < i1) {
-      Un = uC[i0]; SCn = scC[i0];
-      dm0n = ga0[rowC[i0]*16 + c];
-    }
-    for (int i = i0; i < i1; i += 4) {
-      float4 U = Un; float2 SC = SCn;
-      float dm0 = dm0n;
-      if (i+4 < i1) {
-        Un = uC[i+4]; SCn = scC[i+4];
-        dm0n = ga0[rowC[i+4]*16 + c];
-      }
-      float ux = U.x, uy = U.y, uz = U.z, inv_r = U.w;
-      float b2[5];
-      base2_from_u(ux, uy, uz, b2);
-
-      float S1 = h1s[0]*ux + h1s[1]*uy + h1s[2]*uz;
-      float S2 = h2s[0]*b2[0] + h2s[1]*b2[1] + h2s[2]*b2[2]
-               + h2s[3]*b2[3] + h2s[4]*b2[4];
-
-      float dw0 = dm0 * h0c;
-      float dw3 = dm0 * S1;
-      float dw4 = dm0 * S2;
-
-      float Ki = KRADf * inv_r;
-      float tcv = 2.f * SC.y;
-      float sprev = 0.f, s = SC.x, cprev = 1.f, cc = SC.y;
-      float w0 = b0v, w3 = b3v, w4 = b4v;
-      float P = 0.f, Q = 0.f;
-      #pragma unroll
-      for (int k = 0; k < 8; k++) {
-        float rad = Ki * s;
-        w0 += rad*wr0[k]; w3 += rad*wr3[k]; w4 += rad*wr4[k];
-        float t = dw0*wr0[k] + dw3*wr3[k] + dw4*wr4[k];
-        P = fmaf(t*cc, (float)(k+1), P);
-        Q = fmaf(t, rad, Q);
-        float sn = tcv*s - sprev; sprev = s; s = sn;
-        float cn = tcv*cc - cprev; cprev = cc; cc = cn;
-      }
-
-      float t3 = dm0 * w3, t4 = dm0 * w4;
-      accg0 += dm0 * w0;
-      accg1[0] += t3*ux; accg1[1] += t3*uy; accg1[2] += t3*uz;
-      #pragma unroll
-      for (int m = 0; m < 5; m++) accg2[m] += t4*b2[m];
-
-      float q1x = t3*h1s[0], q1y = t3*h1s[1], q1z = t3*h1s[2];
-      float q0 = t4*h2s[0], q1 = t4*h2s[1], q2 = t4*h2s[2], q3 = t4*h2s[3], q4 = t4*h2s[4];
-      float q4d = q4 + q4;
-      float q2h = 6.f*q2;
-      float gr = (KPI5f*P - Q) * inv_r;
-      float gux = q1x + uy*q0 + uz*q3 + ux*q4d;
-      float guy = q1y + ux*q0 + uz*q1 - uy*q4d;
-      float guz = q1z + uy*q1 + uz*q2h + ux*q3;
-
-      gr  = grp16_sum(gr);
-      gux = grp16_sum(gux);
-      guy = grp16_sum(guy);
-      guz = grp16_sum(guz);
-
-      if (c == 0) {
-        float gdotu = gux*ux + guy*uy + guz*uz;
-        dv_col[i*3+0] = gr*ux + (gux - gdotu*ux)*inv_r;
-        dv_col[i*3+1] = gr*uy + (guy - gdotu*uy)*inv_r;
-        dv_col[i*3+2] = gr*uz + (guz - gdotu*uz)*inv_r;
-      }
-    }
-    accg0 = xgrp_sum(accg0);
-    #pragma unroll
-    for (int m = 0; m < 3; m++) accg1[m] = xgrp_sum(accg1[m]);
-    #pragma unroll
-    for (int m = 0; m < 5; m++) accg2[m] = xgrp_sum(accg2[m]);
-    if (g == 0) {
-      g0[n*16 + c] += accg0;
-      g1[n*48 + c*3 + 0] = SQRT3f*accg1[0];
-      g1[n*48 + c*3 + 1] = SQRT3f*accg1[1];
-      g1[n*48 + c*3 + 2] = SQRT3f*accg1[2];
-      g2[n*80 + c*5 + 0] = SQRT15f*accg2[0];
-      g2[n*80 + c*5 + 1] = SQRT15f*accg2[1];
-      g2[n*80 + c*5 + 2] = CSH2f  *accg2[2];
-      g2[n*80 + c*5 + 3] = SQRT15f*accg2[3];
-      g2[n*80 + c*5 + 4] = CSH4f  *accg2[4];
-    }
-  }
-}
-
-__global__ void k_bwd_b0_row(const float* __restrict__ Wr, const float* __restrict__ br,
-                             const float* __restrict__ h0_in,
-                             const float* __restrict__ ga0, const float* __restrict__ ga1,
-                             const float* __restrict__ ga2,
-                             const float4* __restrict__ uR, const float2* __restrict__ scR,
-                             const int* __restrict__ colR,
-                             const int* __restrict__ start_row, const int* __restrict__ deg_row,
-                             float* __restrict__ dv_row, int N)
-{
-  int wid = (blockIdx.x * blockDim.x + threadIdx.x) >> 6;
-  int nw  = (gridDim.x * blockDim.x) >> 6;
-  int lane = threadIdx.x & 63;
-  int g = lane >> 4, c = lane & 15;
-  float wr0[8], wr1[8], wr2[8];
-  #pragma unroll
-  for (int k = 0; k < 8; k++) {
-    wr0[k] = Wr[k*80 + c];
-    wr1[k] = Wr[k*80 + 16 + c];
-    wr2[k] = Wr[k*80 + 32 + c];
-  }
   float b1v = br[16 + c], b2v = br[32 + c];
 
   for (int n = wid; n < N; n += nw) {
@@ -605,17 +625,20 @@
 
     int i0 = start_row[n] + g, i1 = start_row[n] + deg_row[n];
     float4 Un = {0,0,0,0}; float2 SCn = {0,0};
-    float h0n = 0.f;
+    float h0n = 0.f; int cB = 0;
     if (i0 < i1) {
+      int cA = colR[i0];
+      cB = (i0+4 < i1) ? colR[i0+4] : 0;
       Un = uR[i0]; SCn = scR[i0];
-      h0n = h0_in[colR[i0]*16 + c];
+      h0n = h0_in[cA*16 + c];
     }
     for (int i = i0; i < i1; i += 4) {
       float4 U = Un; float2 SC = SCn;
       float h0c = h0n;
       if (i+4 < i1) {
         Un = uR[i+4]; SCn = scR[i+4];
-        h0n = h0_in[colR[i+4]*16 + c];
+        h0n = h0_in[cB*16 + c];
+        cB = (i+8 < i1) ? colR[i+8] : 0;
       }
       float ux = U.x, uy = U.y, uz = U.z, inv_r = U.w;
       float b2[5];
@@ -740,8 +763,6 @@
   float* a2    = f; f += (size_t)N*80;
   float* ga0b1 = f; f += (size_t)N*16;
   float* g0    = f; f += (size_t)N*16;
-  float* g1    = f; f += (size_t)N*48;
-  float* g2    = f; f += (size_t)N*80;
   float* dv_c  = f; f += (size_t)E*3;
   float* dv_r  = f; f += (size_t)E*3;
   float* partials = f; f += (size_t)NB_READOUT;
@@ -774,9 +795,8 @@
   k_node_init<<<cdiv(N, BLK), BLK, 0, stream>>>(emb, z, W_init, h0_s0, N);
 
   k_fwd_b0<<<PBLK, BLK, 0, stream>>>(Wr, br, h0_s0, uR, scR, colR,
-                                     start_row, deg_row, a0, a1, a2, N);
-  k_node_update<<<cdiv(N*16, BLK), BLK, 0, stream>>>(h0_s0, a0, a1, a2,
-                                                     W_out, h0_s1, h1_s1, h2_s1, N);
+                                     start_row, deg_row, W_out,
+                                     h0_s1, h1_s1, h2_s1, N);
 
   k_fwd_b1<<<PBLK, BLK, 0, stream>>>(Wr + 640, br + 80,
                                      h0_s1, h1_s1, h2_s1, uR, scR, colR,
@@ -789,9 +809,8 @@
   k_bwd_b1_col<<<PBLK, BLK, 0, stream>>>(Wr + 640, br + 80,
                                          h0_s1, h1_s1, h2_s1, ga0b1,
                                          uC, scC, rowC, start_col, deg_col,
-                                         g0, g1, g2, dv_c, N);
-
-  k_ga<<<cdiv(N*16, BLK), BLK, 0, stream>>>(g0, g1, g2, W_out, a0, a1, a2, N);
+                                         g0, W_out, a0, a1, a2, dv_c, N);
+
   k_bwd_b0_row<<<PBLK, BLK, 0, stream>>>(Wr, br, h0_s0,
                                          a0, a1, a2, uR, scR, colR,
                                          start_row, deg_row, dv_r, N);
```
